# Kernel optimization log

Hardware: AMD Instinct MI355X
Metric: run time of the kernel (lower is better)

Reference implementation:

```python
import jax, jax.numpy as jnp
import numpy as np

N, IN_DIM, D, H, OUT = 4096, 512, 256, 256, 128


def setup_inputs() -> dict:
    key = jax.random.key(0)
    ks = jax.random.split(key, 12)
    s = 0.05
    x = jax.random.normal(ks[0], (N, IN_DIM), dtype=jnp.float32)
    # sparse-ish dense adjacency mask (avg degree ~80), int since only adj>0 is used
    adj = (jax.random.uniform(ks[1], (N, N)) < 0.02).astype(jnp.int32)
    return {
        "x": x,
        "adj": adj,
        "lin1_w": jax.random.normal(ks[2], (D, IN_DIM), dtype=jnp.float32) * s,
        "lin1_b": jax.random.normal(ks[3], (D,), dtype=jnp.float32) * s,
        "gat_W": jax.random.normal(ks[4], (D, D), dtype=jnp.float32) * s,
        "a_self": jax.random.normal(ks[5], (D,), dtype=jnp.float32) * s,
        "a_neigh": jax.random.normal(ks[6], (D,), dtype=jnp.float32) * s,
        "W_ih": jax.random.normal(ks[7], (4 * H, D), dtype=jnp.float32) * s,
        "W_hh": jax.random.normal(ks[8], (4 * H, H), dtype=jnp.float32) * s,
        "lin2_w": jax.random.normal(ks[9], (OUT, D), dtype=jnp.float32) * s,
        "lin2_b": jax.random.normal(ks[10], (OUT,), dtype=jnp.float32) * s,
    }


def reference(x, adj, lin1_w, lin1_b, gat_W, a_self, a_neigh, W_ih, W_hh, lin2_w, lin2_b):
    M = jnp.float32(0.2)        # scalar M passed by EWNELayer
    LRELU_SLOPE = 0.2           # alpha given to GraphAttentionLayer
    NEG_INF = jnp.float32(-9e15)

    # lin1
    x1 = x @ lin1_w.T + lin1_b                       # [N, D]

    # --- GraphAttentionLayer (DAEGC-style, dense adjacency mask) ---
    h = x1 @ gat_W                                   # [N, D]
    e = (h @ a_self)[:, None] + (h @ a_neigh)[None, :]  # [N, N]
    e = jax.nn.leaky_relu(e * M, LRELU_SLOPE)
    scores = jnp.where(adj > 0, e, NEG_INF)
    attn = jax.nn.softmax(scores, axis=1)            # [N, N]
    h_prime = attn @ h                               # [N, D]
    g = jnp.tanh(jax.nn.elu(h_prime))                # ELU (concat=True) then tanh

    # --- single-timestep LSTM, no bias, h0 = c0 = 0 ---
    h0 = jnp.zeros((N, H), dtype=g.dtype)
    c0 = jnp.zeros((N, H), dtype=g.dtype)
    gates = g @ W_ih.T + h0 @ W_hh.T                 # [N, 4H], torch order i,f,g,o
    i_g, f_g, g_g, o_g = jnp.split(gates, 4, axis=1)
    i_g = jax.nn.sigmoid(i_g)
    f_g = jax.nn.sigmoid(f_g)
    g_g = jnp.tanh(g_g)
    o_g = jax.nn.sigmoid(o_g)
    c1 = f_g * c0 + i_g * g_g
    h1 = o_g * jnp.tanh(c1)                          # [N, H]

    # lin2 -> normalize -> dot-product decode
    out = h1 @ lin2_w.T + lin2_b                     # [N, OUT]
    norm = jnp.maximum(jnp.linalg.norm(out, axis=1, keepdims=True), 1e-12)
    z = out / norm
    A_pred = jax.nn.sigmoid(z @ z.T)                 # [N, N]
    return A_pred, z, out
```

## Files before the change

### kernel.cpp

```cpp
#include <hip/hip_runtime.h>

#define NN_ 4096
#define IN_DIM_ 512
#define D_ 256
#define OUT_ 128

typedef unsigned short u16;
typedef unsigned int u32;
typedef __attribute__((ext_vector_type(8))) short short8;
typedef __attribute__((ext_vector_type(4))) float f32x4;

union U16x8 { uint4 u4; short8 s8; };

__device__ __forceinline__ u16 f2bf(float f){
  u32 u = __builtin_bit_cast(u32, f);
  u = (u + 0x7FFFu + ((u >> 16) & 1u)) >> 16;
  return (u16)u;
}
__device__ __forceinline__ float bf2f(u16 u){ return __builtin_bit_cast(float, ((u32)u) << 16); }
__device__ __forceinline__ float sigm(float v){ return __fdividef(1.f, 1.f + __expf(-v)); }

__device__ __forceinline__ void mfma_mainloop(const u16* __restrict__ A,
    const u16* __restrict__ B, int K, int ldA, int ldB, int row0, int col0,
    uint4* As, uint4* Bs, f32x4 acc[4][4], int tid) {
  const int wave = tid >> 6, lane = tid & 63;
  const int wm = wave >> 1, wn = wave & 1;
  const int r16 = lane & 15, kg = lane >> 4;
  for (int k0 = 0; k0 < K; k0 += 64) {
    #pragma unroll
    for (int i = 0; i < 4; i++) {
      int id = tid + (i << 8);
      int r = id >> 3, cc = id & 7;
      As[(r << 3) + (cc ^ (r & 7))] = *(const uint4*)(A + (size_t)(row0 + r) * ldA + k0 + cc * 8);
      Bs[(r << 3) + (cc ^ (r & 7))] = *(const uint4*)(B + (size_t)(col0 + r) * ldB + k0 + cc * 8);
    }
    __syncthreads();
    #pragma unroll
    for (int ks = 0; ks < 2; ks++) {
      int kb = (ks << 2) + kg;
      U16x8 a[4], b[4];
      #pragma unroll
      for (int m2 = 0; m2 < 4; m2++) {
        int r = (wm << 6) + (m2 << 4) + r16;
        a[m2].u4 = As[(r << 3) + (kb ^ (r & 7))];
      }
      #pragma unroll
      for (int n2 = 0; n2 < 4; n2++) {
        int r = (wn << 6) + (n2 << 4) + r16;
        b[n2].u4 = Bs[(r << 3) + (kb ^ (r & 7))];
      }
      #pragma unroll
      for (int m2 = 0; m2 < 4; m2++)
        #pragma unroll
        for (int n2 = 0; n2 < 4; n2++)
          acc[m2][n2] = __builtin_amdgcn_mfma_f32_16x16x32_bf16(
              a[m2].s8, b[n2].s8, acc[m2][n2], 0, 0, 0);
    }
    __syncthreads();
  }
}

__global__ __launch_bounds__(256) void prep_kernel(
    const float* __restrict__ lin1_w, const float* __restrict__ gat_W,
    const float* __restrict__ lin1_b,
    u16* __restrict__ WcT_bf, float* __restrict__ bcomb) {
  __shared__ __align__(16) float As[32][36];
  __shared__ __align__(16) float Bs[32][36];
  const int b = blockIdx.x, tid = threadIdx.x;
  if (b < 128) {
    const int m0 = (b & 15) << 5;
    const int n0 = (b >> 4) << 5;
    const int tx = tid & 15, ty = tid >> 4;
    float acc[2][2] = {};
    for (int k0 = 0; k0 < 256; k0 += 32) {
      int kk = tid >> 3, c4 = (tid & 7) << 2;
      *(float4*)&As[kk][c4] = *(const float4*)(lin1_w + (size_t)(k0 + kk) * 512 + m0 + c4);
      *(float4*)&Bs[kk][c4] = *(const float4*)(gat_W + (size_t)(k0 + kk) * 256 + n0 + c4);
      __syncthreads();
      #pragma unroll
      for (int k2 = 0; k2 < 32; k2++) {
        float a0 = As[k2][(ty << 1)], a1 = As[k2][(ty << 1) + 1];
        float b0 = Bs[k2][(tx << 1)], b1 = Bs[k2][(tx << 1) + 1];
        acc[0][0] = __builtin_fmaf(a0, b0, acc[0][0]);
        acc[0][1] = __builtin_fmaf(a0, b1, acc[0][1]);
        acc[1][0] = __builtin_fmaf(a1, b0, acc[1][0]);
        acc[1][1] = __builtin_fmaf(a1, b1, acc[1][1]);
      }
      __syncthreads();
    }
    #pragma unroll
    for (int r = 0; r < 2; r++)
      #pragma unroll
      for (int c = 0; c < 2; c++)
        WcT_bf[(size_t)(n0 + (tx << 1) + c) * 512 + m0 + (ty << 1) + r] = f2bf(acc[r][c]);
  } else {
    float a = 0.f;
    #pragma unroll 8
    for (int d = 0; d < 256; d++)
      a = __builtin_fmaf(lin1_b[d], gat_W[(size_t)d * 256 + tid], a);
    bcomb[tid] = a;
  }
}

__global__ __launch_bounds__(256) void hgemm_st_kernel(const float* __restrict__ x,
    const u16* __restrict__ WcT, const float* __restrict__ bias,
    const float* __restrict__ a_self, const float* __restrict__ a_nei,
    const float* __restrict__ W_ih, const float* __restrict__ lin2_w,
    u16* __restrict__ h_bf, float* __restrict__ s, float* __restrict__ t,
    u16* __restrict__ Wihp_bf, u16* __restrict__ l2w_bf) {
  __shared__ uint4 As[16 * 8];
  __shared__ uint4 Bs[256 * 8];
  __shared__ float sred[4][16];
  __shared__ float tred[4][16];
  const int tid = threadIdx.x;
  int b = blockIdx.x;
  if (b >= 256) {
    b -= 256;
    if (b < 192) {
      int r = (b << 2) + (tid >> 6);
      int grp = r / 48, rem = r - grp * 48;
      int gidx = rem >> 4, hcl = rem & 15;
      int gate = (gidx == 0) ? 0 : ((gidx == 1) ? 2 : 3);
      int orig = gate * 256 + grp * 16 + hcl;
      int k = (tid & 63) << 2;
      float4 v = *(const float4*)(W_ih + (size_t)orig * 256 + k);
      ushort4 o = {f2bf(v.x), f2bf(v.y), f2bf(v.z), f2bf(v.w)};
      *(ushort4*)(Wihp_bf + (size_t)r * 256 + k) = o;
    } else {
      int off = (b - 192) * 1024 + tid * 4;
      float4 v = *(const float4*)(lin2_w + off);
      ushort4 o = {f2bf(v.x), f2bf(v.y), f2bf(v.z), f2bf(v.w)};
      *(ushort4*)(l2w_bf + off) = o;
    }
    return;
  }
  const int row0 = b << 4;
  const int wave = tid >> 6, lane = tid & 63;
  const int r16 = lane & 15, kg = lane >> 4;
  f32x4 acc[4];
  #pragma unroll
  for (int n2 = 0; n2 < 4; n2++) acc[n2] = (f32x4){0.f,0.f,0.f,0.f};
  for (int k0 = 0; k0 < IN_DIM_; k0 += 64) {
    if (tid < 128) {
      int r = tid >> 3, cc = tid & 7;
      const float* src = x + (size_t)(row0 + r) * IN_DIM_ + k0 + cc * 8;
      float4 lo = *(const float4*)src;
      float4 hi = *(const float4*)(src + 4);
      u16 e[8] = {f2bf(lo.x), f2bf(lo.y), f2bf(lo.z), f2bf(lo.w),
                  f2bf(hi.x), f2bf(hi.y), f2bf(hi.z), f2bf(hi.w)};
      As[(r << 3) + (cc ^ (r & 7))] = *(uint4*)e;
    }
    #pragma unroll
    for (int i = 0; i < 8; i++) {
      int id = tid + (i << 8);
      int r = id >> 3, cc = id & 7;
      Bs[(r << 3) + (cc ^ (r & 7))] = *(const uint4*)(WcT + (size_t)r * IN_DIM_ + k0 + cc * 8);
    }
    __syncthreads();
    #pragma unroll
    for (int ks = 0; ks < 2; ks++) {
      int kb = (ks << 2) + kg;
      U16x8 a, bb[4];
      a.u4 = As[(r16 << 3) + (kb ^ (r16 & 7))];
      #pragma unroll
      for (int n2 = 0; n2 < 4; n2++) {
        int r = (wave << 6) + (n2 << 4) + r16;
        bb[n2].u4 = Bs[(r << 3) + (kb ^ (r & 7))];
      }
      #pragma unroll
      for (int n2 = 0; n2 < 4; n2++)
        acc[n2] = __builtin_amdgcn_mfma_f32_16x16x32_bf16(a.s8, bb[n2].s8, acc[n2], 0, 0, 0);
    }
    __syncthreads();
  }
  float ps[4] = {0.f,0.f,0.f,0.f}, pt[4] = {0.f,0.f,0.f,0.f};
  #pragma unroll
  for (int n2 = 0; n2 < 4; n2++) {
    int col = (wave << 6) + (n2 << 4) + r16;
    float as = a_self[col], an = a_nei[col], bs = bias[col];
    #pragma unroll
    for (int q = 0; q < 4; q++) {
      float v = acc[n2][q] + bs;
      h_bf[(size_t)(row0 + (kg << 2) + q) * D_ + col] = f2bf(v);
      ps[q] = __builtin_fmaf(v, as, ps[q]);
      pt[q] = __builtin_fmaf(v, an, pt[q]);
    }
  }
  #pragma unroll
  for (int q = 0; q < 4; q++) {
    #pragma unroll
    for (int off = 8; off; off >>= 1) {
      ps[q] += __shfl_xor(ps[q], off);
      pt[q] += __shfl_xor(pt[q], off);
    }
  }
  if (r16 == 0) {
    #pragma unroll
    for (int q = 0; q < 4; q++) {
      sred[wave][(kg << 2) + q] = ps[q];
      tred[wave][(kg << 2) + q] = pt[q];
    }
  }
  __syncthreads();
  if (tid < 16)
    s[row0 + tid] = sred[0][tid] + sred[1][tid] + sred[2][tid] + sred[3][tid];
  else if (tid < 32)
    t[row0 + tid - 16] = tred[0][tid-16] + tred[1][tid-16] + tred[2][tid-16] + tred[3][tid-16];
}

#define MAXN 512
__global__ __launch_bounds__(256) void attn3_kernel(const int* __restrict__ adj,
    const u16* __restrict__ h_bf, const float* __restrict__ s,
    const float* __restrict__ t, u16* __restrict__ g_bf) {
  __shared__ int nidx[MAXN];
  __shared__ float ne[MAXN];
  __shared__ float red[4][256];
  __shared__ int wtot[4];
  __shared__ float reds[4];
  const int tid = threadIdx.x;
  const int row = blockIdx.x;
  const int lane = tid & 63, wave = tid >> 6;
  const int4* arow = (const int4*)(adj + (size_t)row * NN_);
  int4 a4[4];
  #pragma unroll
  for (int i = 0; i < 4; i++) a4[i] = arow[(i << 8) + tid];
  int vals[16] = {a4[0].x, a4[0].y, a4[0].z, a4[0].w, a4[1].x, a4[1].y, a4[1].z, a4[1].w,
                  a4[2].x, a4[2].y, a4[2].z, a4[2].w, a4[3].x, a4[3].y, a4[3].z, a4[3].w};
  f32x4 tv[4];
  #pragma unroll
  for (int i = 0; i < 4; i++) tv[i] = ((const f32x4*)t)[(i << 8) + tid];
  int c = 0;
  #pragma unroll
  for (int q = 0; q < 16; q++) c += (vals[q] > 0);
  int pref = c;
  #pragma unroll
  for (int off = 1; off < 64; off <<= 1) {
    int u = __shfl_up(pref, off);
    if (lane >= off) pref += u;
  }
  if (lane == 63) wtot[wave] = pref;
  __syncthreads();
  int woff = 0;
  #pragma unroll
  for (int w = 0; w < 4; w++) woff += (w < wave) ? wtot[w] : 0;
  int n = wtot[0] + wtot[1] + wtot[2] + wtot[3];
  float si = s[row];
  int p = woff + pref - c;
  float ls = 0.f;
  #pragma unroll
  for (int i = 0; i < 4; i++)
    #pragma unroll
    for (int q = 0; q < 4; q++) {
      if (vals[(i << 2) + q] > 0) {
        int j = (i << 10) + (tid << 2) + q;
        float e = 0.2f * (si + tv[i][q]);
        e = e > 0.f ? e : 0.2f * e;
        float wgt = __expf(e);
        if (p < MAXN) { nidx[p] = j; ne[p] = wgt; ls += wgt; }
        p++;
      }
    }
  if (n > MAXN) n = MAXN;
  #pragma unroll
  for (int off = 32; off; off >>= 1) ls += __shfl_xor(ls, off);
  if (lane == 0) reds[wave] = ls;
  __syncthreads();
  float S = reds[0] + reds[1] + reds[2] + reds[3];
  const int hl = lane & 31, ksel = lane >> 5;
  float acc[8] = {0.f, 0.f, 0.f, 0.f, 0.f, 0.f, 0.f, 0.f};
  #pragma unroll 4
  for (int k = (wave << 1) + ksel; k < n; k += 8) {
    float wgt = ne[k];
    int j = nidx[k];
    U16x8 hv; hv.u4 = *(const uint4*)(h_bf + ((size_t)j << 8) + (hl << 3));
    #pragma unroll
    for (int q = 0; q < 8; q++)
      acc[q] = __builtin_fmaf(wgt, bf2f((u16)hv.s8[q]), acc[q]);
  }
  #pragma unroll
  for (int q = 0; q < 8; q++) acc[q] += __shfl_down(acc[q], 32);
  if (lane < 32) {
    #pragma unroll
    for (int q = 0; q < 8; q++) red[wave][(hl << 3) + q] = acc[q];
  }
  __syncthreads();
  float hp;
  if (n > 0) {
    hp = (red[0][tid] + red[1][tid] + red[2][tid] + red[3][tid]) / S;
  } else {
    float a2 = 0.f;
    for (int j = 0; j < NN_; j++) a2 += bf2f(h_bf[((size_t)j << 8) + tid]);
    hp = a2 / NN_;
  }
  float el = hp > 0.f ? hp : __expf(hp) - 1.f;
  g_bf[((size_t)row << 8) + tid] = f2bf(tanhf(el));
}

__global__ __launch_bounds__(256) void gates_lstm_kernel(const u16* __restrict__ A,
    const u16* __restrict__ B, u16* __restrict__ h1b) {
  __shared__ uint4 As[128 * 8];
  __shared__ uint4 Bs[96 * 8];
  const int tid = threadIdx.x;
  const int row0 = blockIdx.y << 7;
  const int col0 = blockIdx.x * 96;
  const int wave = tid >> 6, lane = tid & 63;
  const int wm = wave >> 1, wn = wave & 1;
  const int r16 = lane & 15, kg = lane >> 4;
  f32x4 acc[4][3];
  #pragma unroll
  for (int m2 = 0; m2 < 4; m2++)
    #pragma unroll
    for (int n2 = 0; n2 < 3; n2++) acc[m2][n2] = (f32x4){0.f,0.f,0.f,0.f};
  for (int k0 = 0; k0 < D_; k0 += 64) {
    #pragma unroll
    for (int i = 0; i < 4; i++) {
      int id = tid + (i << 8);
      int r = id >> 3, cc = id & 7;
      As[(r << 3) + (cc ^ (r & 7))] = *(const uint4*)(A + (size_t)(row0 + r) * D_ + k0 + cc * 8);
    }
    #pragma unroll
    for (int i = 0; i < 3; i++) {
      int id = tid + (i << 8);
      int r = id >> 3, cc = id & 7;
      Bs[(r << 3) + (cc ^ (r & 7))] = *(const uint4*)(B + (size_t)(col0 + r) * D_ + k0 + cc * 8);
    }
    __syncthreads();
    #pragma unroll
    for (int ks = 0; ks < 2; ks++) {
      int kb = (ks << 2) + kg;
      U16x8 a[4], bb[3];
      #pragma unroll
      for (int m2 = 0; m2 < 4; m2++) {
        int r = (wm << 6) + (m2 << 4) + r16;
        a[m2].u4 = As[(r << 3) + (kb ^ (r & 7))];
      }
      #pragma unroll
      for (int n2 = 0; n2 < 3; n2++) {
        int r = wn * 48 + (n2 << 4) + r16;
        bb[n2].u4 = Bs[(r << 3) + (kb ^ (r & 7))];
      }
      #pragma unroll
      for (int m2 = 0; m2 < 4; m2++)
        #pragma unroll
        for (int n2 = 0; n2 < 3; n2++)
          acc[m2][n2] = __builtin_amdgcn_mfma_f32_16x16x32_bf16(
              a[m2].s8, bb[n2].s8, acc[m2][n2], 0, 0, 0);
    }
    __syncthreads();
  }
  const int hc = ((blockIdx.x << 1) + wn) * 16 + r16;
  #pragma unroll
  for (int m2 = 0; m2 < 4; m2++)
    #pragma unroll
    for (int q = 0; q < 4; q++) {
      size_t grow = row0 + (wm << 6) + (m2 << 4) + (kg << 2) + q;
      float ig = acc[m2][0][q], gg = acc[m2][1][q], og = acc[m2][2][q];
      float c1 = sigm(ig) * tanhf(gg);
      h1b[grow * D_ + hc] = f2bf(sigm(og) * tanhf(c1));
    }
}

__global__ __launch_bounds__(256) void lin2f_kernel(const u16* __restrict__ A,
    const u16* __restrict__ B, const float* __restrict__ bias,
    float* __restrict__ out, float* __restrict__ z, u16* __restrict__ zb) {
  __shared__ uint4 As[16 * 8];
  __shared__ uint4 Bs[128 * 8];
  __shared__ float ssred[4][16];
  const int tid = threadIdx.x;
  const int wave = tid >> 6, lane = tid & 63;
  const int r16 = lane & 15, kg = lane >> 4;
  const int row0 = blockIdx.x << 4;
  f32x4 acc[2];
  acc[0] = (f32x4){0.f,0.f,0.f,0.f}; acc[1] = (f32x4){0.f,0.f,0.f,0.f};
  for (int k0 = 0; k0 < D_; k0 += 64) {
    if (tid < 128) {
      int r = tid >> 3, cc = tid & 7;
      As[(r << 3) + (cc ^ (r & 7))] = *(const uint4*)(A + (size_t)(row0 + r) * D_ + k0 + cc * 8);
    }
    #pragma unroll
    for (int i = 0; i < 4; i++) {
      int id = tid + (i << 8);
      int r = id >> 3, cc = id & 7;
      Bs[(r << 3) + (cc ^ (r & 7))] = *(const uint4*)(B + (size_t)r * D_ + k0 + cc * 8);
    }
    __syncthreads();
    #pragma unroll
    for (int ks = 0; ks < 2; ks++) {
      int kb = (ks << 2) + kg;
      U16x8 a, bb[2];
      a.u4 = As[(r16 << 3) + (kb ^ (r16 & 7))];
      #pragma unroll
      for (int n2 = 0; n2 < 2; n2++) {
        int r = (wave << 5) + (n2 << 4) + r16;
        bb[n2].u4 = Bs[(r << 3) + (kb ^ (r & 7))];
      }
      #pragma unroll
      for (int n2 = 0; n2 < 2; n2++)
        acc[n2] = __builtin_amdgcn_mfma_f32_16x16x32_bf16(a.s8, bb[n2].s8, acc[n2], 0, 0, 0);
    }
    __syncthreads();
  }
  float v[2][4], ss[4];
  #pragma unroll
  for (int q = 0; q < 4; q++) ss[q] = 0.f;
  #pragma unroll
  for (int n2 = 0; n2 < 2; n2++) {
    int col = (wave << 5) + (n2 << 4) + r16;
    float bs = bias[col];
    #pragma unroll
    for (int q = 0; q < 4; q++) {
      float vv = acc[n2][q] + bs;
      v[n2][q] = vv;
      ss[q] = __builtin_fmaf(vv, vv, ss[q]);
    }
  }
  #pragma unroll
  for (int q = 0; q < 4; q++)
    #pragma unroll
    for (int off = 8; off; off >>= 1) ss[q] += __shfl_xor(ss[q], off);
  if (r16 == 0) {
    #pragma unroll
    for (int q = 0; q < 4; q++) ssred[wave][(kg << 2) + q] = ss[q];
  }
  __syncthreads();
  #pragma unroll
  for (int q = 0; q < 4; q++) {
    int rrow = (kg << 2) + q;
    float tot = ssred[0][rrow] + ssred[1][rrow] + ssred[2][rrow] + ssred[3][rrow];
    float inv = __fdividef(1.f, fmaxf(sqrtf(tot), 1e-12f));
    size_t grow = row0 + rrow;
    #pragma unroll
    for (int n2 = 0; n2 < 2; n2++) {
      int col = (wave << 5) + (n2 << 4) + r16;
      float vv = v[n2][q], zz = vv * inv;
      out[grow * OUT_ + col] = vv;
      z[grow * OUT_ + col] = zz;
      zb[grow * OUT_ + col] = f2bf(zz);
    }
  }
}

__global__ __launch_bounds__(256) void decode_kernel(const u16* __restrict__ zb,
    float* __restrict__ C) {
  __shared__ uint4 As[128 * 8];
  __shared__ uint4 Bs[128 * 8];
  const int tid = threadIdx.x;
  const int row0 = blockIdx.y << 7, col0 = blockIdx.x << 7;
  f32x4 acc[4][4];
  #pragma unroll
  for (int m2 = 0; m2 < 4; m2++)
    #pragma unroll
    for (int n2 = 0; n2 < 4; n2++) acc[m2][n2] = (f32x4){0.f,0.f,0.f,0.f};
  mfma_mainloop(zb, zb, OUT_, OUT_, OUT_, row0, col0, As, Bs, acc, tid);
  const int wave = tid >> 6, lane = tid & 63;
  const int r16 = lane & 15, kg = lane >> 4;
  const int orow = row0 + ((wave >> 1) << 6), ocol = col0 + ((wave & 1) << 6);
  #pragma unroll
  for (int m2 = 0; m2 < 4; m2++)
    #pragma unroll
    for (int n2 = 0; n2 < 4; n2++)
      #pragma unroll
      for (int q = 0; q < 4; q++) {
        size_t gr = orow + (m2 << 4) + (kg << 2) + q;
        int gc = ocol + (n2 << 4) + r16;
        C[gr * NN_ + gc] = sigm(acc[m2][n2][q]);
      }
}

extern "C" void kernel_launch(void* const* d_in, const int* in_sizes, int n_in,
                              void* d_out, int out_size, void* d_ws, size_t ws_size,
                              hipStream_t stream) {
  const float* x      = (const float*)d_in[0];
  const int*   adj    = (const int*)  d_in[1];
  const float* lin1_w = (const float*)d_in[2];
  const float* lin1_b = (const float*)d_in[3];
  const float* gat_W  = (const float*)d_in[4];
  const float* a_self = (const float*)d_in[5];
  const float* a_nei  = (const float*)d_in[6];
  const float* W_ih   = (const float*)d_in[7];
  const float* lin2_w = (const float*)d_in[9];
  const float* lin2_b = (const float*)d_in[10];

  float* A_pred = (float*)d_out;
  float* z_out  = A_pred + (size_t)NN_ * NN_;
  float* out_o  = z_out + (size_t)NN_ * OUT_;

  char* w = (char*)d_ws;
  u16* h_bf    = (u16*)w;
  u16* g_bf    = (u16*)(w + (2u << 20));
  u16* h1_bf   = (u16*)(w + (4u << 20));
  u16* zb      = (u16*)(w + (6u << 20));
  u16* Wihp_bf = (u16*)(w + (7u << 20));
  u16* WcT_bf  = (u16*)(w + (7u << 20) + (384u << 10));
  u16* l2w_bf  = (u16*)(w + (7u << 20) + (640u << 10));
  float* bcomb = (float*)(w + (7u << 20) + (704u << 10));
  float* s     = (float*)(w + (7u << 20) + (768u << 10));
  float* t     = (float*)(w + (7u << 20) + (832u << 10));

  prep_kernel<<<dim3(129), dim3(256), 0, stream>>>(
      lin1_w, gat_W, lin1_b, WcT_bf, bcomb);
  hgemm_st_kernel<<<dim3(480), dim3(256), 0, stream>>>(
      x, WcT_bf, bcomb, a_self, a_nei, W_ih, lin2_w, h_bf, s, t, Wihp_bf, l2w_bf);
  attn3_kernel<<<dim3(4096), dim3(256), 0, stream>>>(adj, h_bf, s, t, g_bf);
  gates_lstm_kernel<<<dim3(8, 32), dim3(256), 0, stream>>>(g_bf, Wihp_bf, h1_bf);
  lin2f_kernel<<<dim3(256), dim3(256), 0, stream>>>(h1_bf, l2w_bf, lin2_b, out_o, z_out, zb);
  decode_kernel<<<dim3(32, 32), dim3(256), 0, stream>>>(zb, A_pred);
}
```

Measured before the change: 81.57 us.

## Move adjacency compaction into the GEMM kernel to overlap with projection work

The scan of the dense 64MB int adjacency matrix, which builds per-row neighbor index lists, moves out of the attention kernel and into extra blocks of the hgemm kernel. Those blocks run alongside the projection GEMM and write compact u16 neighbor lists plus counts to workspace, using nontemporal loads. The attention kernel then reads only the compact lists and computes the exponentials from t[j] gathers. The neighbor cap drops from 512 to 320 and the attention kernel gains extra global traffic, while the adjacency read is meant to hide behind the GEMM.

```diff
diff --git a/kernel.cpp b/kernel.cpp
--- a/kernel.cpp
+++ b/kernel.cpp
@@ -4,11 +4,13 @@
 #define IN_DIM_ 512
 #define D_ 256
 #define OUT_ 128
+#define MAXC 320
 
 typedef unsigned short u16;
 typedef unsigned int u32;
 typedef __attribute__((ext_vector_type(8))) short short8;
 typedef __attribute__((ext_vector_type(4))) float f32x4;
+typedef __attribute__((ext_vector_type(4))) int i32x4;
 
 union U16x8 { uint4 u4; short8 s8; };
 
@@ -106,14 +108,58 @@
     const u16* __restrict__ WcT, const float* __restrict__ bias,
     const float* __restrict__ a_self, const float* __restrict__ a_nei,
     const float* __restrict__ W_ih, const float* __restrict__ lin2_w,
+    const int* __restrict__ adj,
     u16* __restrict__ h_bf, float* __restrict__ s, float* __restrict__ t,
-    u16* __restrict__ Wihp_bf, u16* __restrict__ l2w_bf) {
+    u16* __restrict__ Wihp_bf, u16* __restrict__ l2w_bf,
+    u16* __restrict__ nidxg, int* __restrict__ cnt) {
   __shared__ uint4 As[16 * 8];
   __shared__ uint4 Bs[256 * 8];
   __shared__ float sred[4][16];
   __shared__ float tred[4][16];
+  __shared__ int wtot4[4];
   const int tid = threadIdx.x;
   int b = blockIdx.x;
+  if (b >= 480) {
+    const int row = b - 480;
+    const int lane = tid & 63, wave = tid >> 6;
+    const i32x4* arow = (const i32x4*)(adj + (size_t)row * NN_);
+    i32x4 a4[4];
+    #pragma unroll
+    for (int i = 0; i < 4; i++) a4[i] = __builtin_nontemporal_load(&arow[(i << 8) + tid]);
+    int vals[16];
+    #pragma unroll
+    for (int i = 0; i < 4; i++)
+      #pragma unroll
+      for (int q = 0; q < 4; q++) vals[(i << 2) + q] = a4[i][q];
+    int c = 0;
+    #pragma unroll
+    for (int q = 0; q < 16; q++) c += (vals[q] > 0);
+    int pref = c;
+    #pragma unroll
+    for (int off = 1; off < 64; off <<= 1) {
+      int u = __shfl_up(pref, off);
+      if (lane >= off) pref += u;
+    }
+    if (lane == 63) wtot4[wave] = pref;
+    __syncthreads();
+    int woff = 0;
+    #pragma unroll
+    for (int w = 0; w < 4; w++) woff += (w < wave) ? wtot4[w] : 0;
+    int n = wtot4[0] + wtot4[1] + wtot4[2] + wtot4[3];
+    int p = woff + pref - c;
+    #pragma unroll
+    for (int i = 0; i < 4; i++)
+      #pragma unroll
+      for (int q = 0; q < 4; q++) {
+        if (vals[(i << 2) + q] > 0) {
+          int j = (i << 10) + (tid << 2) + q;
+          if (p < MAXC) nidxg[(size_t)row * MAXC + p] = (u16)j;
+          p++;
+        }
+      }
+    if (tid == 0) cnt[row] = n;
+    return;
+  }
   if (b >= 256) {
     b -= 256;
     if (b < 192) {
@@ -208,59 +254,28 @@
     t[row0 + tid - 16] = tred[0][tid-16] + tred[1][tid-16] + tred[2][tid-16] + tred[3][tid-16];
 }
 
-#define MAXN 512
-__global__ __launch_bounds__(256) void attn3_kernel(const int* __restrict__ adj,
-    const u16* __restrict__ h_bf, const float* __restrict__ s,
-    const float* __restrict__ t, u16* __restrict__ g_bf) {
-  __shared__ int nidx[MAXN];
-  __shared__ float ne[MAXN];
+__global__ __launch_bounds__(256) void attn4_kernel(const u16* __restrict__ nidxg,
+    const int* __restrict__ cnt, const u16* __restrict__ h_bf,
+    const float* __restrict__ s, const float* __restrict__ t,
+    u16* __restrict__ g_bf) {
+  __shared__ int nidx[MAXC];
+  __shared__ float ne[MAXC];
   __shared__ float red[4][256];
-  __shared__ int wtot[4];
   __shared__ float reds[4];
   const int tid = threadIdx.x;
   const int row = blockIdx.x;
   const int lane = tid & 63, wave = tid >> 6;
-  const int4* arow = (const int4*)(adj + (size_t)row * NN_);
-  int4 a4[4];
-  #pragma unroll
-  for (int i = 0; i < 4; i++) a4[i] = arow[(i << 8) + tid];
-  int vals[16] = {a4[0].x, a4[0].y, a4[0].z, a4[0].w, a4[1].x, a4[1].y, a4[1].z, a4[1].w,
-                  a4[2].x, a4[2].y, a4[2].z, a4[2].w, a4[3].x, a4[3].y, a4[3].z, a4[3].w};
-  f32x4 tv[4];
-  #pragma unroll
-  for (int i = 0; i < 4; i++) tv[i] = ((const f32x4*)t)[(i << 8) + tid];
-  int c = 0;
-  #pragma unroll
-  for (int q = 0; q < 16; q++) c += (vals[q] > 0);
-  int pref = c;
-  #pragma unroll
-  for (int off = 1; off < 64; off <<= 1) {
-    int u = __shfl_up(pref, off);
-    if (lane >= off) pref += u;
-  }
-  if (lane == 63) wtot[wave] = pref;
-  __syncthreads();
-  int woff = 0;
-  #pragma unroll
-  for (int w = 0; w < 4; w++) woff += (w < wave) ? wtot[w] : 0;
-  int n = wtot[0] + wtot[1] + wtot[2] + wtot[3];
-  float si = s[row];
-  int p = woff + pref - c;
+  int n = cnt[row];
+  if (n > MAXC) n = MAXC;
+  const float si = s[row];
   float ls = 0.f;
-  #pragma unroll
-  for (int i = 0; i < 4; i++)
-    #pragma unroll
-    for (int q = 0; q < 4; q++) {
-      if (vals[(i << 2) + q] > 0) {
-        int j = (i << 10) + (tid << 2) + q;
-        float e = 0.2f * (si + tv[i][q]);
-        e = e > 0.f ? e : 0.2f * e;
-        float wgt = __expf(e);
-        if (p < MAXN) { nidx[p] = j; ne[p] = wgt; ls += wgt; }
-        p++;
-      }
-    }
-  if (n > MAXN) n = MAXN;
+  for (int k = tid; k < n; k += 256) {
+    int j = nidxg[(size_t)row * MAXC + k];
+    float e = 0.2f * (si + t[j]);
+    e = e > 0.f ? e : 0.2f * e;
+    float wgt = __expf(e);
+    nidx[k] = j; ne[k] = wgt; ls += wgt;
+  }
   #pragma unroll
   for (int off = 32; off; off >>= 1) ls += __shfl_xor(ls, off);
   if (lane == 0) reds[wave] = ls;
@@ -496,12 +511,15 @@
   float* bcomb = (float*)(w + (7u << 20) + (704u << 10));
   float* s     = (float*)(w + (7u << 20) + (768u << 10));
   float* t     = (float*)(w + (7u << 20) + (832u << 10));
+  u16* nidxg   = (u16*)(w + (8u << 20));
+  int* cnt     = (int*)(w + (11u << 20));
 
   prep_kernel<<<dim3(129), dim3(256), 0, stream>>>(
       lin1_w, gat_W, lin1_b, WcT_bf, bcomb);
-  hgemm_st_kernel<<<dim3(480), dim3(256), 0, stream>>>(
-      x, WcT_bf, bcomb, a_self, a_nei, W_ih, lin2_w, h_bf, s, t, Wihp_bf, l2w_bf);
-  attn3_kernel<<<dim3(4096), dim3(256), 0, stream>>>(adj, h_bf, s, t, g_bf);
+  hgemm_st_kernel<<<dim3(4576), dim3(256), 0, stream>>>(
+      x, WcT_bf, bcomb, a_self, a_nei, W_ih, lin2_w, adj,
+      h_bf, s, t, Wihp_bf, l2w_bf, nidxg, cnt);
+  attn4_kernel<<<dim3(4096), dim3(256), 0, stream>>>(nidxg, cnt, h_bf, s, t, g_bf);
   gates_lstm_kernel<<<dim3(8, 32), dim3(256), 0, stream>>>(g_bf, Wihp_bf, h1_bf);
   lin2f_kernel<<<dim3(256), dim3(256), 0, stream>>>(h1_bf, l2w_bf, lin2_b, out_o, z_out, zb);
   decode_kernel<<<dim3(32, 32), dim3(256), 0, stream>>>(zb, A_pred);
```

After: 80.09 us, median of 2. Within noise of the previous version (-1.8%).
